# Optimization experiments

Measured on AMD Instinct MI355X. Metric: run time of the kernel, lower is better.

The kernel has to match this reference:

```python
import jax, jax.numpy as jnp
import numpy as np

N = 50000
E = 800000
IN_CH = 128
HID = 64
OUT_CH = 1
HEADS = 2


def setup_inputs() -> dict:
    key = jax.random.key(0)
    k1, k2, k3, k4, k5, k6, k7 = jax.random.split(key, 7)
    x = jax.random.normal(k1, (N, IN_CH), dtype=jnp.float32)
    row = jax.random.randint(k2, (E,), 0, N)
    col = jax.random.randint(k3, (E,), 0, N)
    edge_index = jnp.stack([row, col], axis=0).astype(jnp.int64)
    # Xavier-uniform-ish init scales
    def xavier(k, shape):
        fan_in, fan_out = shape[0], shape[1]
        lim = float(np.sqrt(6.0 / (fan_in + fan_out)))
        return jax.random.uniform(k, shape, jnp.float32, -lim, lim)
    W0 = xavier(k4, (IN_CH, HEADS * HID))          # layer 0 lin weight (transposed torch layout)
    attn0 = xavier(k5, (HEADS, 2 * HID))
    W1 = xavier(k6, (HID, HEADS * OUT_CH))         # layer 1 lin weight
    attn1 = xavier(k7, (HEADS, 2 * OUT_CH))
    return {"x": x, "edge_index": edge_index, "W0": W0, "attn0": attn0, "W1": W1, "attn1": attn1}


def _segment_softmax(alpha, row, num_nodes):
    # alpha: [E, H]; per-target-node (row) softmax across incoming edges.
    m = jax.ops.segment_max(alpha, row, num_segments=num_nodes)   # [N, H]
    ex = jnp.exp(alpha - m[row])
    s = jax.ops.segment_sum(ex, row, num_segments=num_nodes)      # [N, H]
    return ex / s[row]


def _gat_layer(x, edge_index, W, attn, heads, out_ch):
    n = x.shape[0]
    h = (x @ W).reshape(n, heads, out_ch)                         # [N, H, C]
    row, col = edge_index[0], edge_index[1]
    h_row = h[row]                                                # [E, H, C]
    h_col = h[col]                                                # [E, H, C]
    # (cat([h_row,h_col]) * attn).sum(-1) split into two contractions
    alpha = (jnp.einsum('ehc,hc->eh', h_row, attn[:, :out_ch])
             + jnp.einsum('ehc,hc->eh', h_col, attn[:, out_ch:]))
    alpha = jax.nn.leaky_relu(alpha, negative_slope=0.2)
    alpha = _segment_softmax(alpha, row, n)                        # [E, H]
    out = jax.ops.segment_sum(alpha[..., None] * h_col, row, num_segments=n)  # [N, H, C]
    return out.mean(axis=1), alpha


def reference(x, edge_index, W0, attn0, W1, attn1):
    h, _ = _gat_layer(x, edge_index, W0, attn0, HEADS, HID)
    h = jax.nn.relu(h)
    out, attn = _gat_layer(h, edge_index, W1, attn1, HEADS, OUT_CH)
    return out  # [N, OUT_CH]
```

## Files before the change

kernel.cpp:

```cpp
#include <hip/hip_runtime.h>
#include <math.h>

#define NNODES 50000
#define NEDGES 800000
#define NBKT 196
#define BKT_CAP 5120
#define EPB 2048
#define NBA ((NEDGES + EPB - 1) / EPB)
#define NBN ((NNODES + 63) / 64)

typedef __attribute__((ext_vector_type(8))) short short8;
typedef __attribute__((ext_vector_type(4))) float f32x4;

__device__ inline float bsum64(float v) {
    #pragma unroll
    for (int off = 1; off < 64; off <<= 1) v += __shfl_xor(v, off, 64);
    return v;
}

__device__ inline unsigned packbf2(float a, float b) {
    unsigned ua = __float_as_uint(a);
    unsigned ub = __float_as_uint(b);
    ua = (ua + 0x7fffu + ((ua >> 16) & 1u)) >> 16;
    ub = (ub + 0x7fffu + ((ub >> 16) & 1u)) >> 16;
    return ua | (ub << 16);
}
__device__ inline float bflo(unsigned u) { return __uint_as_float(u << 16); }
__device__ inline float bfhi(unsigned u) { return __uint_as_float(u & 0xffff0000u); }

__global__ __launch_bounds__(256) void k_prep(const float* __restrict__ W,
                                              unsigned short* __restrict__ Whi,
                                              unsigned short* __restrict__ Wlo,
                                              int* __restrict__ gcur) {
    if (blockIdx.x == 64) {
        int i = threadIdx.x;
        if (i < NBKT) gcur[i] = 0;
        return;
    }
    int tid = blockIdx.x * 256 + threadIdx.x;
    int i = tid & 7, lane = (tid >> 3) & 63, ct = (tid >> 9) & 7, kc = tid >> 12;
    int k = kc * 32 + (lane >> 4) * 8 + i;
    int col = ct * 16 + (lane & 15);
    float v = W[k * 128 + col];
    unsigned hb = packbf2(v, 0.f) & 0xffffu;
    float hv = __uint_as_float(hb << 16);
    unsigned lb = packbf2(v - hv, 0.f) & 0xffffu;
    Whi[tid] = (unsigned short)hb;
    Wlo[tid] = (unsigned short)lb;
}

__global__ __launch_bounds__(256) void k_nodeA(const int* __restrict__ ei,
                                               int* __restrict__ gcur,
                                               unsigned* __restrict__ stag,
                                               const float* __restrict__ x,
                                               const unsigned short* __restrict__ Whi,
                                               const unsigned short* __restrict__ Wlo,
                                               const float* __restrict__ attn0,
                                               float* __restrict__ ar,
                                               float* __restrict__ ac,
                                               unsigned* __restrict__ h0b) {
    __shared__ int lh[NBKT];
    __shared__ int lbase[NBKT];
    int t = threadIdx.x;

    if (blockIdx.x < NBA) {
        for (int i = t; i < NBKT; i += 256) lh[i] = 0;
        __syncthreads();
        int e0 = blockIdx.x * EPB;
        int rows[8], cols[8];
        #pragma unroll
        for (int i = 0; i < 8; i++) {
            int e = e0 + i * 256 + t;
            if (e < NEDGES) {
                rows[i] = ei[e];
                cols[i] = ei[NEDGES + e];
                atomicAdd(&lh[rows[i] >> 8], 1);
            }
        }
        __syncthreads();
        for (int i = t; i < NBKT; i += 256) {
            lbase[i] = atomicAdd(&gcur[i], lh[i]);
            lh[i] = 0;
        }
        __syncthreads();
        #pragma unroll
        for (int i = 0; i < 8; i++) {
            int e = e0 + i * 256 + t;
            if (e < NEDGES) {
                int b = rows[i] >> 8;
                int rank = atomicAdd(&lh[b], 1);
                stag[b * BKT_CAP + lbase[b] + rank] =
                    ((unsigned)(rows[i] & 255) << 16) | (unsigned)cols[i];
            }
        }
        return;
    }

    int bid = blockIdx.x - NBA;
    int w = t >> 6, lane = t & 63;
    int n0 = bid * 64 + w * 16;
    int c16 = lane & 15, grp = lane >> 4;
    int arow = n0 + c16;
    bool rowok = arow < NNODES;

    f32x4 acc[8];
    #pragma unroll
    for (int ct = 0; ct < 8; ct++) acc[ct] = (f32x4){0.f, 0.f, 0.f, 0.f};

    const uint4* WH = (const uint4*)Whi;
    const uint4* WL = (const uint4*)Wlo;

    for (int kc = 0; kc < 4; kc++) {
        float xv[8];
        if (rowok) {
            *(float4*)&xv[0] = *(const float4*)&x[arow * 128 + kc * 32 + grp * 8];
            *(float4*)&xv[4] = *(const float4*)&x[arow * 128 + kc * 32 + grp * 8 + 4];
        } else {
            #pragma unroll
            for (int i = 0; i < 8; i++) xv[i] = 0.f;
        }
        unsigned ah[4];
        #pragma unroll
        for (int i = 0; i < 4; i++) ah[i] = packbf2(xv[2 * i], xv[2 * i + 1]);
        short8 a_h = *(short8*)ah;

        #pragma unroll
        for (int ct = 0; ct < 8; ct++) {
            uint4 whv = WH[(kc * 8 + ct) * 64 + lane];
            uint4 wlv = WL[(kc * 8 + ct) * 64 + lane];
            short8 b_h = *(short8*)&whv;
            short8 b_l = *(short8*)&wlv;
            acc[ct] = __builtin_amdgcn_mfma_f32_16x16x32_bf16(a_h, b_h, acc[ct], 0, 0, 0);
            acc[ct] = __builtin_amdgcn_mfma_f32_16x16x32_bf16(a_h, b_l, acc[ct], 0, 0, 0);
        }
    }

    #pragma unroll
    for (int reg = 0; reg < 4; reg++) {
        float pr0 = 0.f, pc0 = 0.f, pr1 = 0.f, pc1 = 0.f;
        #pragma unroll
        for (int ct = 0; ct < 4; ct++) {
            float v = acc[ct][reg];
            int ch = ct * 16 + c16;
            pr0 += v * attn0[ch];
            pc0 += v * attn0[64 + ch];
        }
        #pragma unroll
        for (int ct = 4; ct < 8; ct++) {
            float v = acc[ct][reg];
            int ch = (ct - 4) * 16 + c16;
            pr1 += v * attn0[128 + ch];
            pc1 += v * attn0[192 + ch];
        }
        #pragma unroll
        for (int off = 1; off < 16; off <<= 1) {
            pr0 += __shfl_xor(pr0, off, 64);
            pc0 += __shfl_xor(pc0, off, 64);
            pr1 += __shfl_xor(pr1, off, 64);
            pc1 += __shfl_xor(pc1, off, 64);
        }
        int n = n0 + grp * 4 + reg;
        if (c16 == 0 && n < NNODES) {
            ar[n * 2] = pr0;     ac[n * 2] = pc0;
            ar[n * 2 + 1] = pr1; ac[n * 2 + 1] = pc1;
        }
    }

    #pragma unroll
    for (int reg = 0; reg < 4; reg++) {
        int n = n0 + grp * 4 + reg;
        if (n < NNODES) {
            #pragma unroll
            for (int ct = 0; ct < 4; ct++)
                h0b[n * 64 + ct * 16 + c16] = packbf2(acc[ct][reg], acc[ct + 4][reg]);
        }
    }
}

__global__ __launch_bounds__(256) void k_binC(const int* __restrict__ gcur,
                                              const unsigned* __restrict__ stag,
                                              int* __restrict__ rowptr,
                                              int* __restrict__ ecol) {
    __shared__ int sh[256];
    __shared__ int dg[256];
    __shared__ int sc[256];
    __shared__ int cur[256];
    __shared__ int lout[BKT_CAP];
    int b = blockIdx.x, t = threadIdx.x;
    int gv = (t < NBKT) ? gcur[t] : 0;
    sh[t] = gv;
    __syncthreads();
    #pragma unroll
    for (int off = 1; off < 256; off <<= 1) {
        int u = (t >= off) ? sh[t - off] : 0;
        __syncthreads();
        sh[t] += u;
        __syncthreads();
    }
    int cnt = gcur[b];
    int base = sh[b] - cnt;
    dg[t] = 0;
    __syncthreads();
    for (int i = t; i < cnt; i += 256)
        atomicAdd(&dg[stag[b * BKT_CAP + i] >> 16], 1);
    __syncthreads();
    int v = dg[t];
    sc[t] = v;
    __syncthreads();
    #pragma unroll
    for (int off = 1; off < 256; off <<= 1) {
        int u = (t >= off) ? sc[t - off] : 0;
        __syncthreads();
        sc[t] += u;
        __syncthreads();
    }
    int excl = sc[t] - v;
    int gidx = b * 256 + t;
    if (gidx <= NNODES) rowptr[gidx] = base + excl;
    cur[t] = excl;
    __syncthreads();
    for (int i = t; i < cnt; i += 256) {
        unsigned p = stag[b * BKT_CAP + i];
        int pos = atomicAdd(&cur[p >> 16], 1);
        lout[pos] = (int)(p & 0xffffu);
    }
    __syncthreads();
    for (int i = t; i < cnt; i += 256) ecol[base + i] = lout[i];
}

__global__ __launch_bounds__(256) void k_l0edge(const int* __restrict__ rowptr,
                                                const int* __restrict__ ecol,
                                                const float* __restrict__ ar,
                                                const float* __restrict__ ac,
                                                const unsigned* __restrict__ h0b,
                                                const float* __restrict__ W1,
                                                float* __restrict__ h1) {
    int w = threadIdx.x >> 6, lane = threadIdx.x & 63;
    int n = blockIdx.x * 4 + w;
    if (n >= NNODES) return;
    int beg = rowptr[n];
    int deg = rowptr[n + 1] - beg;
    float arn0 = ar[n * 2], arn1 = ar[n * 2 + 1];
    int esub = lane >> 4;
    int c16 = lane & 15;
    float accA[4] = {0.f, 0.f, 0.f, 0.f};
    float accB[4] = {0.f, 0.f, 0.f, 0.f};
    float s0t = 0.f, s1t = 0.f;
    for (int wb = 0; wb < deg; wb += 64) {
        int cnt = deg - wb; if (cnt > 64) cnt = 64;
        float p0 = 0.f, p1 = 0.f; int colr = 0;
        if (lane < cnt) {
            colr = ecol[beg + wb + lane];
            float2 acv = ((const float2*)ac)[colr];
            float a0 = arn0 + acv.x, a1 = arn1 + acv.y;
            a0 = a0 > 0.f ? a0 : 0.2f * a0;
            a1 = a1 > 0.f ? a1 : 0.2f * a1;
            p0 = __expf(a0); p1 = __expf(a1);
            s0t += p0; s1t += p1;
        }
        int tmax = (cnt + 3) >> 2;
        for (int tt = 0; tt < tmax; tt++) {
            int i4 = tt * 4 + esub;
            int colx = __shfl(colr, i4, 64);
            float q0 = __shfl(p0, i4, 64);
            float q1 = __shfl(p1, i4, 64);
            if (i4 < cnt) {
                const uint4 u = *(const uint4*)(h0b + colx * 64 + c16 * 4);
                accA[0] += q0 * bflo(u.x); accB[0] += q1 * bfhi(u.x);
                accA[1] += q0 * bflo(u.y); accB[1] += q1 * bfhi(u.y);
                accA[2] += q0 * bflo(u.z); accB[2] += q1 * bfhi(u.z);
                accA[3] += q0 * bflo(u.w); accB[3] += q1 * bfhi(u.w);
            }
        }
    }
    float s0 = bsum64(s0t), s1 = bsum64(s1t);
    #pragma unroll
    for (int jj = 0; jj < 4; jj++) {
        accA[jj] += __shfl_xor(accA[jj], 16, 64);
        accA[jj] += __shfl_xor(accA[jj], 32, 64);
        accB[jj] += __shfl_xor(accB[jj], 16, 64);
        accB[jj] += __shfl_xor(accB[jj], 32, 64);
    }
    float si0 = deg ? 0.5f / s0 : 0.f;
    float si1 = deg ? 0.5f / s1 : 0.f;
    float pA = 0.f, pB = 0.f;
    #pragma unroll
    for (int jj = 0; jj < 4; jj++) {
        float o = si0 * accA[jj] + si1 * accB[jj];
        o = o > 0.f ? o : 0.f;
        float2 wv = ((const float2*)W1)[c16 * 4 + jj];
        pA += o * wv.x; pB += o * wv.y;
    }
    #pragma unroll
    for (int off = 1; off < 16; off <<= 1) {
        pA += __shfl_xor(pA, off, 64);
        pB += __shfl_xor(pB, off, 64);
    }
    if (lane == 0) { h1[n * 2] = pA; h1[n * 2 + 1] = pB; }
}

__global__ __launch_bounds__(256) void k_fused1(const int* __restrict__ rowptr,
                                                const int* __restrict__ ecol,
                                                const float* __restrict__ h1,
                                                const float* __restrict__ attn1,
                                                float* __restrict__ dout) {
    int w = threadIdx.x >> 6, lane = threadIdx.x & 63;
    int n = blockIdx.x * 4 + w;
    if (n >= NNODES) return;
    int beg = rowptr[n], end = rowptr[n + 1];
    if (beg == end) { if (lane == 0) dout[n] = 0.f; return; }
    float w01 = attn1[1], w11 = attn1[3];
    float base0 = attn1[0] * h1[n * 2];
    float base1 = attn1[2] * h1[n * 2 + 1];
    float s0 = 0.f, s1 = 0.f, acc0 = 0.f, acc1 = 0.f;
    for (int i = beg + lane; i < end; i += 64) {
        int col = ecol[i];
        float2 v = ((const float2*)h1)[col];
        float a0 = base0 + w01 * v.x;
        float a1 = base1 + w11 * v.y;
        a0 = a0 > 0.f ? a0 : 0.2f * a0;
        a1 = a1 > 0.f ? a1 : 0.2f * a1;
        float p0 = __expf(a0), p1 = __expf(a1);
        s0 += p0; acc0 += p0 * v.x;
        s1 += p1; acc1 += p1 * v.y;
    }
    s0 = bsum64(s0); s1 = bsum64(s1);
    acc0 = bsum64(acc0); acc1 = bsum64(acc1);
    if (lane == 0) dout[n] = 0.5f * (acc0 / s0 + acc1 / s1);
}

extern "C" void kernel_launch(void* const* d_in, const int* in_sizes, int n_in,
                              void* d_out, int out_size, void* d_ws, size_t ws_size,
                              hipStream_t stream) {
    const float* x     = (const float*)d_in[0];
    const int*   ei    = (const int*)d_in[1];
    const float* W0    = (const float*)d_in[2];
    const float* attn0 = (const float*)d_in[3];
    const float* W1    = (const float*)d_in[4];
    const float* attn1 = (const float*)d_in[5];
    float* dout = (float*)d_out;

    float* ws = (float*)d_ws;
    float*          ar     = ws;
    float*          ac     = ar + NNODES * 2;
    float*          h1     = ac + NNODES * 2;
    unsigned*       h0b    = (unsigned*)(h1 + NNODES * 2);
    unsigned short* Whi    = (unsigned short*)(h0b + NNODES * 64);
    unsigned short* Wlo    = Whi + 128 * 128;
    int*            gcur   = (int*)(Wlo + 128 * 128);
    int*            rowptr = gcur + NBKT;
    unsigned*       stag   = (unsigned*)(rowptr + NNODES + 1);
    int*            ecol   = (int*)(stag + NBKT * BKT_CAP);

    k_prep<<<65, 256, 0, stream>>>(W0, Whi, Wlo, gcur);
    k_nodeA<<<NBA + NBN, 256, 0, stream>>>(ei, gcur, stag, x, Whi, Wlo, attn0, ar, ac, h0b);
    k_binC<<<NBKT, 256, 0, stream>>>(gcur, stag, rowptr, ecol);
    k_l0edge<<<(NNODES + 3) / 4, 256, 0, stream>>>(rowptr, ecol, ar, ac, h0b, W1, h1);
    k_fused1<<<(NNODES + 3) / 4, 256, 0, stream>>>(rowptr, ecol, h1, attn1, dout);
}
```

Measured before the change: 98.27 us.

## Regroup kernels to co-schedule bucket scatter with weight prep and CSR build with GEMM

The launch sequence is restructured. The bucket-scatter pass now shares a launch with the weight bf16 split. The per-bucket CSR build runs in the same launch as the node GEMM, with block-index dispatch. The gcur zeroing moves to a hipMemsetAsync. The layer-0 edge gather loop is unrolled by two so two neighbour rows are loaded before accumulating. This aims to overlap independent stages and raise memory-level parallelism, but the GEMM blocks now take the CSR blocks' large shared-memory allocation, which may lower occupancy.

```diff
diff --git a/kernel.cpp b/kernel.cpp
--- a/kernel.cpp
+++ b/kernel.cpp
@@ -8,6 +8,7 @@
 #define EPB 2048
 #define NBA ((NEDGES + EPB - 1) / EPB)
 #define NBN ((NNODES + 63) / 64)
+#define NWP 64
 
 typedef __attribute__((ext_vector_type(8))) short short8;
 typedef __attribute__((ext_vector_type(4))) float f32x4;
@@ -28,75 +29,124 @@
 __device__ inline float bflo(unsigned u) { return __uint_as_float(u << 16); }
 __device__ inline float bfhi(unsigned u) { return __uint_as_float(u & 0xffff0000u); }
 
-__global__ __launch_bounds__(256) void k_prep(const float* __restrict__ W,
-                                              unsigned short* __restrict__ Whi,
-                                              unsigned short* __restrict__ Wlo,
-                                              int* __restrict__ gcur) {
-    if (blockIdx.x == 64) {
-        int i = threadIdx.x;
-        if (i < NBKT) gcur[i] = 0;
+__global__ __launch_bounds__(256) void k_prepA(const float* __restrict__ W,
+                                               unsigned short* __restrict__ Whi,
+                                               unsigned short* __restrict__ Wlo,
+                                               const int* __restrict__ ei,
+                                               int* __restrict__ gcur,
+                                               unsigned* __restrict__ stag) {
+    int t = threadIdx.x;
+    if (blockIdx.x < NWP) {
+        int tid = blockIdx.x * 256 + t;
+        int i = tid & 7, lane = (tid >> 3) & 63, ct = (tid >> 9) & 7, kc = tid >> 12;
+        int k = kc * 32 + (lane >> 4) * 8 + i;
+        int col = ct * 16 + (lane & 15);
+        float v = W[k * 128 + col];
+        unsigned hb = packbf2(v, 0.f) & 0xffffu;
+        float hv = __uint_as_float(hb << 16);
+        unsigned lb = packbf2(v - hv, 0.f) & 0xffffu;
+        Whi[tid] = (unsigned short)hb;
+        Wlo[tid] = (unsigned short)lb;
         return;
     }
-    int tid = blockIdx.x * 256 + threadIdx.x;
-    int i = tid & 7, lane = (tid >> 3) & 63, ct = (tid >> 9) & 7, kc = tid >> 12;
-    int k = kc * 32 + (lane >> 4) * 8 + i;
-    int col = ct * 16 + (lane & 15);
-    float v = W[k * 128 + col];
-    unsigned hb = packbf2(v, 0.f) & 0xffffu;
-    float hv = __uint_as_float(hb << 16);
-    unsigned lb = packbf2(v - hv, 0.f) & 0xffffu;
-    Whi[tid] = (unsigned short)hb;
-    Wlo[tid] = (unsigned short)lb;
-}
-
-__global__ __launch_bounds__(256) void k_nodeA(const int* __restrict__ ei,
-                                               int* __restrict__ gcur,
-                                               unsigned* __restrict__ stag,
-                                               const float* __restrict__ x,
+    __shared__ int lh[NBKT];
+    __shared__ int lbase[NBKT];
+    int blk = blockIdx.x - NWP;
+    for (int i = t; i < NBKT; i += 256) lh[i] = 0;
+    __syncthreads();
+    int e0 = blk * EPB;
+    int rows[8], cols[8];
+    #pragma unroll
+    for (int i = 0; i < 8; i++) {
+        int e = e0 + i * 256 + t;
+        if (e < NEDGES) {
+            rows[i] = ei[e];
+            cols[i] = ei[NEDGES + e];
+            atomicAdd(&lh[rows[i] >> 8], 1);
+        }
+    }
+    __syncthreads();
+    for (int i = t; i < NBKT; i += 256) {
+        lbase[i] = atomicAdd(&gcur[i], lh[i]);
+        lh[i] = 0;
+    }
+    __syncthreads();
+    #pragma unroll
+    for (int i = 0; i < 8; i++) {
+        int e = e0 + i * 256 + t;
+        if (e < NEDGES) {
+            int b = rows[i] >> 8;
+            int rank = atomicAdd(&lh[b], 1);
+            stag[b * BKT_CAP + lbase[b] + rank] =
+                ((unsigned)(rows[i] & 255) << 16) | (unsigned)cols[i];
+        }
+    }
+}
+
+__global__ __launch_bounds__(256) void k_nodeC(const float* __restrict__ x,
                                                const unsigned short* __restrict__ Whi,
                                                const unsigned short* __restrict__ Wlo,
                                                const float* __restrict__ attn0,
                                                float* __restrict__ ar,
                                                float* __restrict__ ac,
-                                               unsigned* __restrict__ h0b) {
-    __shared__ int lh[NBKT];
-    __shared__ int lbase[NBKT];
+                                               unsigned* __restrict__ h0b,
+                                               const int* __restrict__ gcur,
+                                               const unsigned* __restrict__ stag,
+                                               int* __restrict__ rowptr,
+                                               int* __restrict__ ecol) {
+    __shared__ int shmem[256 * 4 + BKT_CAP];
     int t = threadIdx.x;
 
-    if (blockIdx.x < NBA) {
-        for (int i = t; i < NBKT; i += 256) lh[i] = 0;
-        __syncthreads();
-        int e0 = blockIdx.x * EPB;
-        int rows[8], cols[8];
-        #pragma unroll
-        for (int i = 0; i < 8; i++) {
-            int e = e0 + i * 256 + t;
-            if (e < NEDGES) {
-                rows[i] = ei[e];
-                cols[i] = ei[NEDGES + e];
-                atomicAdd(&lh[rows[i] >> 8], 1);
-            }
-        }
-        __syncthreads();
-        for (int i = t; i < NBKT; i += 256) {
-            lbase[i] = atomicAdd(&gcur[i], lh[i]);
-            lh[i] = 0;
-        }
-        __syncthreads();
-        #pragma unroll
-        for (int i = 0; i < 8; i++) {
-            int e = e0 + i * 256 + t;
-            if (e < NEDGES) {
-                int b = rows[i] >> 8;
-                int rank = atomicAdd(&lh[b], 1);
-                stag[b * BKT_CAP + lbase[b] + rank] =
-                    ((unsigned)(rows[i] & 255) << 16) | (unsigned)cols[i];
-            }
-        }
+    if (blockIdx.x >= NBN) {
+        int b = blockIdx.x - NBN;
+        int* sh = shmem;
+        int* dg = sh + 256;
+        int* sc = dg + 256;
+        int* cur = sc + 256;
+        int* lout = cur + 256;
+        int gv = (t < NBKT) ? gcur[t] : 0;
+        sh[t] = gv;
+        __syncthreads();
+        #pragma unroll
+        for (int off = 1; off < 256; off <<= 1) {
+            int u = (t >= off) ? sh[t - off] : 0;
+            __syncthreads();
+            sh[t] += u;
+            __syncthreads();
+        }
+        int cnt = gcur[b];
+        int base = sh[b] - cnt;
+        dg[t] = 0;
+        __syncthreads();
+        for (int i = t; i < cnt; i += 256)
+            atomicAdd(&dg[stag[b * BKT_CAP + i] >> 16], 1);
+        __syncthreads();
+        int v = dg[t];
+        sc[t] = v;
+        __syncthreads();
+        #pragma unroll
+        for (int off = 1; off < 256; off <<= 1) {
+            int u = (t >= off) ? sc[t - off] : 0;
+            __syncthreads();
+            sc[t] += u;
+            __syncthreads();
+        }
+        int excl = sc[t] - v;
+        int gidx = b * 256 + t;
+        if (gidx <= NNODES) rowptr[gidx] = base + excl;
+        cur[t] = excl;
+        __syncthreads();
+        for (int i = t; i < cnt; i += 256) {
+            unsigned p = stag[b * BKT_CAP + i];
+            int pos = atomicAdd(&cur[p >> 16], 1);
+            lout[pos] = (int)(p & 0xffffu);
+        }
+        __syncthreads();
+        for (int i = t; i < cnt; i += 256) ecol[base + i] = lout[i];
         return;
     }
 
-    int bid = blockIdx.x - NBA;
+    int bid = blockIdx.x;
     int w = t >> 6, lane = t & 63;
     int n0 = bid * 64 + w * 16;
     int c16 = lane & 15, grp = lane >> 4;
@@ -175,57 +225,6 @@
                 h0b[n * 64 + ct * 16 + c16] = packbf2(acc[ct][reg], acc[ct + 4][reg]);
         }
     }
-}
-
-__global__ __launch_bounds__(256) void k_binC(const int* __restrict__ gcur,
-                                              const unsigned* __restrict__ stag,
-                                              int* __restrict__ rowptr,
-                                              int* __restrict__ ecol) {
-    __shared__ int sh[256];
-    __shared__ int dg[256];
-    __shared__ int sc[256];
-    __shared__ int cur[256];
-    __shared__ int lout[BKT_CAP];
-    int b = blockIdx.x, t = threadIdx.x;
-    int gv = (t < NBKT) ? gcur[t] : 0;
-    sh[t] = gv;
-    __syncthreads();
-    #pragma unroll
-    for (int off = 1; off < 256; off <<= 1) {
-        int u = (t >= off) ? sh[t - off] : 0;
-        __syncthreads();
-        sh[t] += u;
-        __syncthreads();
-    }
-    int cnt = gcur[b];
-    int base = sh[b] - cnt;
-    dg[t] = 0;
-    __syncthreads();
-    for (int i = t; i < cnt; i += 256)
-        atomicAdd(&dg[stag[b * BKT_CAP + i] >> 16], 1);
-    __syncthreads();
-    int v = dg[t];
-    sc[t] = v;
-    __syncthreads();
-    #pragma unroll
-    for (int off = 1; off < 256; off <<= 1) {
-        int u = (t >= off) ? sc[t - off] : 0;
-        __syncthreads();
-        sc[t] += u;
-        __syncthreads();
-    }
-    int excl = sc[t] - v;
-    int gidx = b * 256 + t;
-    if (gidx <= NNODES) rowptr[gidx] = base + excl;
-    cur[t] = excl;
-    __syncthreads();
-    for (int i = t; i < cnt; i += 256) {
-        unsigned p = stag[b * BKT_CAP + i];
-        int pos = atomicAdd(&cur[p >> 16], 1);
-        lout[pos] = (int)(p & 0xffffu);
-    }
-    __syncthreads();
-    for (int i = t; i < cnt; i += 256) ecol[base + i] = lout[i];
 }
 
 __global__ __launch_bounds__(256) void k_l0edge(const int* __restrict__ rowptr,
@@ -259,18 +258,33 @@
             s0t += p0; s1t += p1;
         }
         int tmax = (cnt + 3) >> 2;
-        for (int tt = 0; tt < tmax; tt++) {
-            int i4 = tt * 4 + esub;
-            int colx = __shfl(colr, i4, 64);
-            float q0 = __shfl(p0, i4, 64);
-            float q1 = __shfl(p1, i4, 64);
-            if (i4 < cnt) {
-                const uint4 u = *(const uint4*)(h0b + colx * 64 + c16 * 4);
-                accA[0] += q0 * bflo(u.x); accB[0] += q1 * bfhi(u.x);
-                accA[1] += q0 * bflo(u.y); accB[1] += q1 * bfhi(u.y);
-                accA[2] += q0 * bflo(u.z); accB[2] += q1 * bfhi(u.z);
-                accA[3] += q0 * bflo(u.w); accB[3] += q1 * bfhi(u.w);
-            }
+        int tt = 0;
+        for (; tt + 2 <= tmax; tt += 2) {
+            int ia = tt * 4 + esub, ib = ia + 4;
+            int colA = __shfl(colr, ia, 64);
+            int colB = __shfl(colr, ib, 64);
+            float qa0 = __shfl(p0, ia, 64), qa1 = __shfl(p1, ia, 64);
+            float qb0 = __shfl(p0, ib, 64), qb1 = __shfl(p1, ib, 64);
+            const uint4 uA = *(const uint4*)(h0b + colA * 64 + c16 * 4);
+            const uint4 uB = *(const uint4*)(h0b + colB * 64 + c16 * 4);
+            accA[0] += qa0 * bflo(uA.x); accB[0] += qa1 * bfhi(uA.x);
+            accA[1] += qa0 * bflo(uA.y); accB[1] += qa1 * bfhi(uA.y);
+            accA[2] += qa0 * bflo(uA.z); accB[2] += qa1 * bfhi(uA.z);
+            accA[3] += qa0 * bflo(uA.w); accB[3] += qa1 * bfhi(uA.w);
+            accA[0] += qb0 * bflo(uB.x); accB[0] += qb1 * bfhi(uB.x);
+            accA[1] += qb0 * bflo(uB.y); accB[1] += qb1 * bfhi(uB.y);
+            accA[2] += qb0 * bflo(uB.z); accB[2] += qb1 * bfhi(uB.z);
+            accA[3] += qb0 * bflo(uB.w); accB[3] += qb1 * bfhi(uB.w);
+        }
+        if (tt < tmax) {
+            int ia = tt * 4 + esub;
+            int colA = __shfl(colr, ia, 64);
+            float qa0 = __shfl(p0, ia, 64), qa1 = __shfl(p1, ia, 64);
+            const uint4 uA = *(const uint4*)(h0b + colA * 64 + c16 * 4);
+            accA[0] += qa0 * bflo(uA.x); accB[0] += qa1 * bfhi(uA.x);
+            accA[1] += qa0 * bflo(uA.y); accB[1] += qa1 * bfhi(uA.y);
+            accA[2] += qa0 * bflo(uA.z); accB[2] += qa1 * bfhi(uA.z);
+            accA[3] += qa0 * bflo(uA.w); accB[3] += qa1 * bfhi(uA.w);
         }
     }
     float s0 = bsum64(s0t), s1 = bsum64(s1t);
@@ -352,9 +366,10 @@
     unsigned*       stag   = (unsigned*)(rowptr + NNODES + 1);
     int*            ecol   = (int*)(stag + NBKT * BKT_CAP);
 
-    k_prep<<<65, 256, 0, stream>>>(W0, Whi, Wlo, gcur);
-    k_nodeA<<<NBA + NBN, 256, 0, stream>>>(ei, gcur, stag, x, Whi, Wlo, attn0, ar, ac, h0b);
-    k_binC<<<NBKT, 256, 0, stream>>>(gcur, stag, rowptr, ecol);
+    hipMemsetAsync(gcur, 0, NBKT * sizeof(int), stream);
+    k_prepA<<<NWP + NBA, 256, 0, stream>>>(W0, Whi, Wlo, ei, gcur, stag);
+    k_nodeC<<<NBN + NBKT, 256, 0, stream>>>(x, Whi, Wlo, attn0, ar, ac, h0b,
+                                            gcur, stag, rowptr, ecol);
     k_l0edge<<<(NNODES + 3) / 4, 256, 0, stream>>>(rowptr, ecol, ar, ac, h0b, W1, h1);
     k_fused1<<<(NNODES + 3) / 4, 256, 0, stream>>>(rowptr, ecol, h1, attn1, dout);
 }
```

Measured after the change: 91.75 us. 6.6% less time.
